# Kernel tuning notes

Measured on AMD Instinct MI355X. Metric: run time of the kernel, lower is better.

Reference implementation:

```python
import jax, jax.numpy as jnp
import numpy as np

EPS = 1e-6

def _rmsnorm(x, w):
    var = jnp.mean(x * x, axis=-1, keepdims=True)
    return w * (x * jax.lax.rsqrt(var + EPS))

def _rope(t, cos, sin):
    # t: [B,S,H,d_k]; cos/sin: [S,d_k/2] -> complex multiply on (even,odd) pairs
    B, S, H, D = t.shape
    tr = t.reshape(B, S, H, D // 2, 2)
    t0, t1 = tr[..., 0], tr[..., 1]
    c = cos[None, :, None, :]
    s = sin[None, :, None, :]
    o0 = t0 * c - t1 * s
    o1 = t0 * s + t1 * c
    return jnp.stack([o0, o1], axis=-1).reshape(B, S, H, D)

def setup_inputs() -> dict:
    key = jax.random.key(0)
    ks = jax.random.split(key, 9)
    B, S, D, H, DFF = 1, 4096, 1024, 16, 4096
    dk = D // H
    hidden = int(2 * DFF / 3)  # 2730, SwiGLU hidden dim
    sc = 0.02
    x = jax.random.normal(ks[0], (B, S, D), jnp.float32)
    # RoPE tables (theta=10000)
    inv_freq = 1.0 / (10000.0 ** (np.arange(0, dk, 2, dtype=np.float32) / dk))
    ang = np.outer(np.arange(S, dtype=np.float32), inv_freq)
    freqs_cos = jnp.asarray(np.cos(ang))
    freqs_sin = jnp.asarray(np.sin(ang))
    # causal additive mask [1,1,S,S]
    mask = jnp.where(np.tril(np.ones((S, S), bool)), 0.0, -1e9).astype(jnp.float32)[None, None]
    Wq = jax.random.normal(ks[1], (D, D), jnp.float32) * sc
    Wk = jax.random.normal(ks[2], (D, D), jnp.float32) * sc
    Wv = jax.random.normal(ks[3], (D, D), jnp.float32) * sc
    Wo = jax.random.normal(ks[4], (D, D), jnp.float32) * sc
    ln1_w = jnp.ones((D,), jnp.float32)
    ln2_w = jnp.ones((D,), jnp.float32)
    w1 = jax.random.normal(ks[5], (D, hidden), jnp.float32) * sc
    w2 = jax.random.normal(ks[6], (hidden, D), jnp.float32) * sc
    w3 = jax.random.normal(ks[7], (D, hidden), jnp.float32) * sc
    return dict(x=x, freqs_cos=freqs_cos, freqs_sin=freqs_sin, mask=mask,
                Wq=Wq, Wk=Wk, Wv=Wv, Wo=Wo, ln1_w=ln1_w, ln2_w=ln2_w,
                w1=w1, w2=w2, w3=w3)

def reference(x, freqs_cos, freqs_sin, mask, Wq, Wk, Wv, Wo, ln1_w, ln2_w, w1, w2, w3):
    B, S, D = x.shape
    H = 16
    dk = D // H
    scale = jnp.sqrt(jnp.float32(dk))
    # attention sublayer (pre-RMSNorm)
    h = _rmsnorm(x, ln1_w)
    Q = (h @ Wq).reshape(B, S, H, dk)
    K = (h @ Wk).reshape(B, S, H, dk)
    V = (h @ Wv).reshape(B, S, H, dk)
    Q = _rope(Q, freqs_cos, freqs_sin)
    K = _rope(K, freqs_cos, freqs_sin)
    scores = jnp.einsum('bshd,bthd->bhst', Q, K) / scale + mask  # [B,H,S,S]
    attn = jax.nn.softmax(scores, axis=-1)
    ctx = jnp.einsum('bhst,bthd->bshd', attn, V).reshape(B, S, D)
    x = x + ctx @ Wo
    # SwiGLU FFN sublayer
    h2 = _rmsnorm(x, ln2_w)
    ff = (jax.nn.silu(h2 @ w1) * (h2 @ w3)) @ w2
    x = x + ff
    return x
```

## Files before the change

### kernel.cpp

```cpp
#include <hip/hip_runtime.h>

#define S_LEN 4096
#define D_MODEL 1024
#define NHEAD 16
#define DK 64
#define HID 2730
#define HIDP 2816
#define QKV_LD 3072

typedef unsigned short u16;
typedef unsigned int u32;
typedef __bf16 bf16x8 __attribute__((ext_vector_type(8)));
typedef float f32x4 __attribute__((ext_vector_type(4)));

#define MFMA16 __builtin_amdgcn_mfma_f32_16x16x32_bf16

__device__ __forceinline__ float b2f(u16 u) {
    return __builtin_bit_cast(float, (u32)u << 16);
}
__device__ __forceinline__ u16 f2b(float f) {
    u32 u = __builtin_bit_cast(u32, f);
    u += 0x7FFF + ((u >> 16) & 1);
    return (u16)(u >> 16);
}
__device__ __forceinline__ u32 pk_trunc(float lo, float hi) {
    return __builtin_amdgcn_perm(__builtin_bit_cast(u32, hi),
                                 __builtin_bit_cast(u32, lo), 0x07060302u);
}
__device__ __forceinline__ void gll16(const u16* g, u16* l) {
    __builtin_amdgcn_global_load_lds(
        (__attribute__((address_space(1))) void*)(g),
        (__attribute__((address_space(3))) void*)(l),
        16, 0, 0);
}

__global__ __launch_bounds__(256)
void rmsnorm_k(const float* __restrict__ x, const float* __restrict__ w,
               u16* __restrict__ out) {
    const int row = blockIdx.x;
    const int tid = threadIdx.x;
    const float4 v = ((const float4*)(x + (size_t)row * D_MODEL))[tid];
    float ss = v.x * v.x + v.y * v.y + v.z * v.z + v.w * v.w;
    for (int o = 32; o; o >>= 1) ss += __shfl_down(ss, o);
    __shared__ float red[4];
    if ((tid & 63) == 0) red[tid >> 6] = ss;
    __syncthreads();
    const float tot = red[0] + red[1] + red[2] + red[3];
    const float rs = rsqrtf(tot * (1.0f / D_MODEL) + 1e-6f);
    const float4 wv = ((const float4*)w)[tid];
    u16* op = out + (size_t)row * D_MODEL + tid * 4;
    u32 p0 = (u32)f2b(v.x * rs * wv.x) | ((u32)f2b(v.y * rs * wv.y) << 16);
    u32 p1 = (u32)f2b(v.z * rs * wv.z) | ((u32)f2b(v.w * rs * wv.w) << 16);
    uint2 pk; pk.x = p0; pk.y = p1;
    *(uint2*)op = pk;
}

__global__ __launch_bounds__(256)
void tcast_k(const float* __restrict__ in, int R, int C,
             u16* __restrict__ out, int outC) {
    __shared__ float t[32][33];
    const int r0 = blockIdx.y * 32;
    const int c0 = blockIdx.x * 32;
    const int tx = threadIdx.x, ty = threadIdx.y;
#pragma unroll
    for (int j = 0; j < 4; ++j) {
        int ir = c0 + ty + j * 8;
        int ic = r0 + tx;
        t[ty + j * 8][tx] = (ir < R && ic < C) ? in[(size_t)ir * C + ic] : 0.0f;
    }
    __syncthreads();
#pragma unroll
    for (int j = 0; j < 4; ++j)
        out[(size_t)(r0 + ty + j * 8) * outC + c0 + tx] = f2b(t[tx][ty + j * 8]);
}

__global__ __launch_bounds__(256)
void packkv_k(const u16* __restrict__ qkv, u16* __restrict__ vt,
              u16* __restrict__ kp) {
    __shared__ u16 t[32][33];
    const int h = blockIdx.z;
    const int t0 = blockIdx.x * 32;
    const int d0 = blockIdx.y * 32;
    const int tx = threadIdx.x, ty = threadIdx.y;
#pragma unroll
    for (int j = 0; j < 4; ++j) {
        const int s = t0 + ty + j * 8;
        t[ty + j * 8][tx] = qkv[(size_t)s * QKV_LD + 2 * D_MODEL + h * DK + d0 + tx];
        kp[((size_t)h * S_LEN + s) * DK + d0 + tx] =
            qkv[(size_t)s * QKV_LD + D_MODEL + h * DK + d0 + tx];
    }
    __syncthreads();
#pragma unroll
    for (int j = 0; j < 4; ++j)
        vt[(size_t)h * DK * S_LEN + (size_t)(d0 + ty + j * 8) * S_LEN + t0 + tx] =
            t[tx][ty + j * 8];
}

__global__ __launch_bounds__(256)
void rope_k(u16* __restrict__ qkv, const float* __restrict__ fc,
            const float* __restrict__ fs) {
    const int idx = blockIdx.x * 256 + threadIdx.x;
    const int s = idx >> 9;
    const int rem = idx & 511;
    const int h = rem >> 5;
    const int i = rem & 31;
    const size_t base = (size_t)s * QKV_LD + h * DK + 2 * i;
    const float c = fc[s * 32 + i], sn = fs[s * 32 + i];
    const float SC = 0.125f * 1.44269504f;
    u16* q = qkv + base;
    u16* k = qkv + base + D_MODEL;
    float t0 = b2f(q[0]), t1 = b2f(q[1]);
    q[0] = f2b((t0 * c - t1 * sn) * SC);
    q[1] = f2b((t0 * sn + t1 * c) * SC);
    t0 = b2f(k[0]); t1 = b2f(k[1]);
    k[0] = f2b(t0 * c - t1 * sn);
    k[1] = f2b(t0 * sn + t1 * c);
}

template <int EPI>
__global__ __launch_bounds__(256)
void gemm128(const u16* __restrict__ A, int lda, const u16* __restrict__ Bt, int ldb,
             void* __restrict__ C, int ldc, int K, const float* __restrict__ resid) {
    const int m0 = blockIdx.y * 128, n0 = blockIdx.x * 128;
    const int tid = threadIdx.x;
    const int wave = tid >> 6, lane = tid & 63;
    const int wr = wave >> 1, wc = wave & 1;
    const int r16 = lane & 15, kq = lane >> 4;

    __shared__ __align__(16) u16 As[128 * 32];
    __shared__ __align__(16) u16 Bs[128 * 32];

    const int srow = tid >> 2, sk = (tid & 3) * 8;
    const u16* ag0 = A + (size_t)(m0 + srow) * lda + sk;
    const u16* ag1 = A + (size_t)(m0 + 64 + srow) * lda + sk;
    const u16* bg0 = Bt + (size_t)(n0 + srow) * ldb + sk;
    const u16* bg1 = Bt + (size_t)(n0 + 64 + srow) * ldb + sk;
    u16* asw = As + wave * 512;
    u16* bsw = Bs + wave * 512;

    f32x4 acc[16];
#pragma unroll
    for (int i = 0; i < 16; ++i) acc[i] = f32x4{0.f, 0.f, 0.f, 0.f};

    for (int k0 = 0; k0 < K; k0 += 32) {
        __syncthreads();
        gll16(ag0 + k0, asw);
        gll16(ag1 + k0, asw + 2048);
        gll16(bg0 + k0, bsw);
        gll16(bg1 + k0, bsw + 2048);
        __syncthreads();
        bf16x8 af[4], bf[4];
#pragma unroll
        for (int mt = 0; mt < 4; ++mt)
            af[mt] = *(const bf16x8*)&As[(wr * 64 + mt * 16 + r16) * 32 + kq * 8];
#pragma unroll
        for (int nt = 0; nt < 4; ++nt)
            bf[nt] = *(const bf16x8*)&Bs[(wc * 64 + nt * 16 + r16) * 32 + kq * 8];
#pragma unroll
        for (int mt = 0; mt < 4; ++mt)
#pragma unroll
            for (int nt = 0; nt < 4; ++nt)
                acc[mt * 4 + nt] = MFMA16(af[mt], bf[nt], acc[mt * 4 + nt], 0, 0, 0);
    }

#pragma unroll
    for (int mt = 0; mt < 4; ++mt) {
#pragma unroll
        for (int nt = 0; nt < 4; ++nt) {
            const int col = n0 + wc * 64 + nt * 16 + r16;
#pragma unroll
            for (int j = 0; j < 4; ++j) {
                const int row = m0 + wr * 64 + mt * 16 + kq * 4 + j;
                if (EPI == 0) {
                    ((u16*)C)[(size_t)row * ldc + col] = f2b(acc[mt * 4 + nt][j]);
                } else {
                    ((float*)C)[(size_t)row * ldc + col] =
                        resid[(size_t)row * ldc + col] + acc[mt * 4 + nt][j];
                }
            }
        }
    }
}

__global__ __launch_bounds__(256)
void gemm64r(const u16* __restrict__ A, int lda, const u16* __restrict__ Bt, int ldb,
             float* __restrict__ C, int ldc, int K, const float* __restrict__ resid) {
    const int m0 = blockIdx.y * 128, n0 = blockIdx.x * 64;
    const int tid = threadIdx.x;
    const int wave = tid >> 6, lane = tid & 63;
    const int r16 = lane & 15, kq = lane >> 4;

    __shared__ __align__(16) u16 As[128 * 32];
    __shared__ __align__(16) u16 Bs[64 * 32];

    const int srow = tid >> 2, sk = (tid & 3) * 8;
    const u16* ag0 = A + (size_t)(m0 + srow) * lda + sk;
    const u16* ag1 = A + (size_t)(m0 + 64 + srow) * lda + sk;
    const u16* bg = Bt + (size_t)(n0 + srow) * ldb + sk;
    u16* asw = As + wave * 512;
    u16* bsw = Bs + wave * 512;

    f32x4 acc[8];
#pragma unroll
    for (int i = 0; i < 8; ++i) acc[i] = f32x4{0.f, 0.f, 0.f, 0.f};

    for (int k0 = 0; k0 < K; k0 += 32) {
        __syncthreads();
        gll16(ag0 + k0, asw);
        gll16(ag1 + k0, asw + 2048);
        gll16(bg + k0, bsw);
        __syncthreads();
        bf16x8 af[2], bf[4];
#pragma unroll
        for (int mt = 0; mt < 2; ++mt)
            af[mt] = *(const bf16x8*)&As[(wave * 32 + mt * 16 + r16) * 32 + kq * 8];
#pragma unroll
        for (int nt = 0; nt < 4; ++nt)
            bf[nt] = *(const bf16x8*)&Bs[(nt * 16 + r16) * 32 + kq * 8];
#pragma unroll
        for (int mt = 0; mt < 2; ++mt)
#pragma unroll
            for (int nt = 0; nt < 4; ++nt)
                acc[mt * 4 + nt] = MFMA16(af[mt], bf[nt], acc[mt * 4 + nt], 0, 0, 0);
    }

#pragma unroll
    for (int mt = 0; mt < 2; ++mt)
#pragma unroll
        for (int nt = 0; nt < 4; ++nt) {
            const int col = n0 + nt * 16 + r16;
#pragma unroll
            for (int j = 0; j < 4; ++j) {
                const int row = m0 + wave * 32 + mt * 16 + kq * 4 + j;
                C[(size_t)row * ldc + col] =
                    resid[(size_t)row * ldc + col] + acc[mt * 4 + nt][j];
            }
        }
}

__global__ __launch_bounds__(256)
void gemm_dual64(const u16* __restrict__ A, int lda,
                 const u16* __restrict__ B1, const u16* __restrict__ B3, int ldb,
                 u16* __restrict__ C, int ldc, int K) {
    const int m0 = blockIdx.y * 128, n0 = blockIdx.x * 64;
    const int tid = threadIdx.x;
    const int wave = tid >> 6, lane = tid & 63;
    const int r16 = lane & 15, kq = lane >> 4;

    __shared__ __align__(16) u16 As[128 * 32];
    __shared__ __align__(16) u16 B1s[64 * 32];
    __shared__ __align__(16) u16 B3s[64 * 32];

    const int srow = tid >> 2, sk = (tid & 3) * 8;
    const u16* ag0 = A + (size_t)(m0 + srow) * lda + sk;
    const u16* ag1 = A + (size_t)(m0 + 64 + srow) * lda + sk;
    const u16* b1g = B1 + (size_t)(n0 + srow) * ldb + sk;
    const u16* b3g = B3 + (size_t)(n0 + srow) * ldb + sk;
    u16* asw = As + wave * 512;
    u16* b1w = B1s + wave * 512;
    u16* b3w = B3s + wave * 512;

    f32x4 acc1[8], acc3[8];
#pragma unroll
    for (int i = 0; i < 8; ++i) {
        acc1[i] = f32x4{0.f, 0.f, 0.f, 0.f};
        acc3[i] = f32x4{0.f, 0.f, 0.f, 0.f};
    }

    for (int k0 = 0; k0 < K; k0 += 32) {
        __syncthreads();
        gll16(ag0 + k0, asw);
        gll16(ag1 + k0, asw + 2048);
        gll16(b1g + k0, b1w);
        gll16(b3g + k0, b3w);
        __syncthreads();
        bf16x8 af[2], b1f[4], b3f[4];
#pragma unroll
        for (int mt = 0; mt < 2; ++mt)
            af[mt] = *(const bf16x8*)&As[(wave * 32 + mt * 16 + r16) * 32 + kq * 8];
#pragma unroll
        for (int nt = 0; nt < 4; ++nt) {
            b1f[nt] = *(const bf16x8*)&B1s[(nt * 16 + r16) * 32 + kq * 8];
            b3f[nt] = *(const bf16x8*)&B3s[(nt * 16 + r16) * 32 + kq * 8];
        }
#pragma unroll
        for (int mt = 0; mt < 2; ++mt)
#pragma unroll
            for (int nt = 0; nt < 4; ++nt) {
                acc1[mt * 4 + nt] = MFMA16(af[mt], b1f[nt], acc1[mt * 4 + nt], 0, 0, 0);
                acc3[mt * 4 + nt] = MFMA16(af[mt], b3f[nt], acc3[mt * 4 + nt], 0, 0, 0);
            }
    }

#pragma unroll
    for (int mt = 0; mt < 2; ++mt)
#pragma unroll
        for (int nt = 0; nt < 4; ++nt) {
            const int col = n0 + nt * 16 + r16;
#pragma unroll
            for (int j = 0; j < 4; ++j) {
                const int row = m0 + wave * 32 + mt * 16 + kq * 4 + j;
                const float v1 = acc1[mt * 4 + nt][j];
                const float v3 = acc3[mt * 4 + nt][j];
                const float sig = 1.0f / (1.0f + __expf(-v1));
                C[(size_t)row * ldc + col] = f2b(v1 * sig * v3);
            }
        }
}

__global__ __launch_bounds__(256)
void flash_k(const u16* __restrict__ qkv, const u16* __restrict__ vt,
             const u16* __restrict__ kp, u16* __restrict__ ctx) {
    const int h = blockIdx.x;
    const int by = blockIdx.y;
    const int hi = by >> 4, lo = by & 15;
    const int base = lo + ((hi >> 1) << 4);
    const int qi = (hi & 1) ? (63 - base) : base;
    const int q0 = qi * 64;
    const int tid = threadIdx.x;
    const int wave = tid >> 6, lane = tid & 63;
    const int r16 = lane & 15, kq = lane >> 4;

    __shared__ __align__(16) u16 Ks[64 * 64];
    __shared__ __align__(16) u16 Vs[64 * 64];
    __shared__ __align__(16) u16 Ps[4][16][72];

    const u16* kb = kp + (size_t)h * S_LEN * DK;
    const u16* vbase = vt + (size_t)h * DK * S_LEN;
    const int srow = tid >> 3;
    const int lcol = ((tid & 7) ^ (srow & 7)) * 8;
    const int qloc = wave * 16 + r16;
    const int sw = r16 & 7;

    const u16* qrow = qkv + (size_t)(q0 + qloc) * QKV_LD + h * DK;
    const bf16x8 qf0 = *(const bf16x8*)(qrow + kq * 8);
    const bf16x8 qf1 = *(const bf16x8*)(qrow + 32 + kq * 8);

    f32x4 o[4];
#pragma unroll
    for (int i = 0; i < 4; ++i) o[i] = f32x4{0.f, 0.f, 0.f, 0.f};
    float lpart = 0.f;

    const int c0 = (kq ^ sw) * 8;
    const int c1 = ((4 ^ kq) ^ sw) * 8;

    for (int t = 0; t <= qi; ++t) {
        const int t0 = t * 64;
        __syncthreads();
#pragma unroll
        for (int i = 0; i < 2; ++i) {
            const int r = srow + i * 32;
            gll16(kb + (size_t)(t0 + r) * DK + lcol, Ks + tid * 8 + i * 2048);
            gll16(vbase + (size_t)r * S_LEN + t0 + lcol, Vs + tid * 8 + i * 2048);
        }
        __syncthreads();

        f32x4 s[4];
#pragma unroll
        for (int nt = 0; nt < 4; ++nt) {
            s[nt] = f32x4{0.f, 0.f, 0.f, 0.f};
            const bf16x8 k0 = *(const bf16x8*)&Ks[(nt * 16 + r16) * 64 + c0];
            s[nt] = MFMA16(k0, qf0, s[nt], 0, 0, 0);
            const bf16x8 k1 = *(const bf16x8*)&Ks[(nt * 16 + r16) * 64 + c1];
            s[nt] = MFMA16(k1, qf1, s[nt], 0, 0, 0);
        }

        float p[16];
#pragma unroll
        for (int nt = 0; nt < 4; ++nt)
#pragma unroll
            for (int j = 0; j < 4; ++j) p[nt * 4 + j] = exp2f(s[nt][j]);
        if (t == qi) {
#pragma unroll
            for (int nt = 0; nt < 4; ++nt)
#pragma unroll
                for (int j = 0; j < 4; ++j)
                    if ((nt * 16 + kq * 4 + j) > qloc) p[nt * 4 + j] = 0.f;
        }
#pragma unroll
        for (int i = 0; i < 16; ++i) lpart += p[i];

#pragma unroll
        for (int nt = 0; nt < 4; ++nt) {
            uint2 pk;
            pk.x = pk_trunc(p[nt * 4 + 0], p[nt * 4 + 1]);
            pk.y = pk_trunc(p[nt * 4 + 2], p[nt * 4 + 3]);
            *(uint2*)&Ps[wave][r16][nt * 16 + kq * 4] = pk;
        }

#pragma unroll
        for (int ks = 0; ks < 2; ++ks) {
            const bf16x8 pf = *(const bf16x8*)&Ps[wave][r16][ks * 32 + kq * 8];
            const int cv = (((ks << 2) ^ kq) ^ sw) * 8;
#pragma unroll
            for (int nt = 0; nt < 4; ++nt) {
                const bf16x8 vf = *(const bf16x8*)&Vs[(nt * 16 + r16) * 64 + cv];
                o[nt] = MFMA16(vf, pf, o[nt], 0, 0, 0);
            }
        }
    }

    lpart += __shfl_xor(lpart, 16);
    lpart += __shfl_xor(lpart, 32);
    const float inv = 1.0f / lpart;
    const size_t row = q0 + qloc;
#pragma unroll
    for (int nt = 0; nt < 4; ++nt) {
        uint2 pk;
        pk.x = (u32)f2b(o[nt][0] * inv) | ((u32)f2b(o[nt][1] * inv) << 16);
        pk.y = (u32)f2b(o[nt][2] * inv) | ((u32)f2b(o[nt][3] * inv) << 16);
        *(uint2*)&ctx[row * D_MODEL + h * DK + nt * 16 + kq * 4] = pk;
    }
}

extern "C" void kernel_launch(void* const* d_in, const int* in_sizes, int n_in,
                              void* d_out, int out_size, void* d_ws, size_t ws_size,
                              hipStream_t stream) {
    const float* x    = (const float*)d_in[0];
    const float* fcos = (const float*)d_in[1];
    const float* fsin = (const float*)d_in[2];
    const float* Wq = (const float*)d_in[4];
    const float* Wk = (const float*)d_in[5];
    const float* Wv = (const float*)d_in[6];
    const float* Wo = (const float*)d_in[7];
    const float* ln1 = (const float*)d_in[8];
    const float* ln2 = (const float*)d_in[9];
    const float* w1 = (const float*)d_in[10];
    const float* w2 = (const float*)d_in[11];
    const float* w3 = (const float*)d_in[12];
    float* out = (float*)d_out;

    char* ws = (char*)d_ws;
    size_t off = 0;
    auto alloc = [&](size_t bytes) -> char* {
        char* p = ws + off;
        off += (bytes + 255) & ~(size_t)255;
        return p;
    };
    u16* hb    = (u16*)alloc((size_t)S_LEN * D_MODEL * 2);
    u16* wqkvt = (u16*)alloc((size_t)QKV_LD * D_MODEL * 2);
    u16* wot   = (u16*)alloc((size_t)D_MODEL * D_MODEL * 2);
    u16* qkvb  = (u16*)alloc((size_t)S_LEN * QKV_LD * 2);
    u16* vt    = (u16*)alloc((size_t)S_LEN * D_MODEL * 2);
    u16* kpack = (u16*)alloc((size_t)S_LEN * D_MODEL * 2);
    u16* ctxb  = (u16*)alloc((size_t)S_LEN * D_MODEL * 2);
    float* x2  = (float*)alloc((size_t)S_LEN * D_MODEL * 4);
    u16* h2b   = (u16*)alloc((size_t)S_LEN * D_MODEL * 2);
    u16* w1t   = (u16*)alloc((size_t)HIDP * D_MODEL * 2);
    u16* w3t   = (u16*)alloc((size_t)HIDP * D_MODEL * 2);
    u16* w2t   = (u16*)alloc((size_t)D_MODEL * HIDP * 2);
    u16* ffb   = (u16*)alloc((size_t)S_LEN * HIDP * 2);

    const dim3 tb32(32, 8);

    tcast_k<<<dim3(32, 32), tb32, 0, stream>>>(Wq, D_MODEL, D_MODEL, wqkvt, D_MODEL);
    tcast_k<<<dim3(32, 32), tb32, 0, stream>>>(Wk, D_MODEL, D_MODEL,
                                               wqkvt + (size_t)D_MODEL * D_MODEL, D_MODEL);
    tcast_k<<<dim3(32, 32), tb32, 0, stream>>>(Wv, D_MODEL, D_MODEL,
                                               wqkvt + (size_t)2 * D_MODEL * D_MODEL, D_MODEL);
    tcast_k<<<dim3(32, 32), tb32, 0, stream>>>(Wo, D_MODEL, D_MODEL, wot, D_MODEL);
    tcast_k<<<dim3(32, HIDP / 32), tb32, 0, stream>>>(w1, D_MODEL, HID, w1t, D_MODEL);
    tcast_k<<<dim3(32, HIDP / 32), tb32, 0, stream>>>(w3, D_MODEL, HID, w3t, D_MODEL);
    tcast_k<<<dim3(HIDP / 32, 32), tb32, 0, stream>>>(w2, HID, D_MODEL, w2t, HIDP);

    rmsnorm_k<<<S_LEN, 256, 0, stream>>>(x, ln1, hb);

    gemm128<0><<<dim3(QKV_LD / 128, S_LEN / 128), 256, 0, stream>>>(
        hb, D_MODEL, wqkvt, D_MODEL, qkvb, QKV_LD, D_MODEL, nullptr);

    rope_k<<<(S_LEN * NHEAD * 32) / 256, 256, 0, stream>>>(qkvb, fcos, fsin);

    packkv_k<<<dim3(S_LEN / 32, DK / 32, NHEAD), tb32, 0, stream>>>(qkvb, vt, kpack);

    flash_k<<<dim3(NHEAD, 64), 256, 0, stream>>>(qkvb, vt, kpack, ctxb);

    gemm64r<<<dim3(D_MODEL / 64, S_LEN / 128), 256, 0, stream>>>(
        ctxb, D_MODEL, wot, D_MODEL, x2, D_MODEL, D_MODEL, x);

    rmsnorm_k<<<S_LEN, 256, 0, stream>>>(x2, ln2, h2b);

    gemm_dual64<<<dim3(HIDP / 64, S_LEN / 128), 256, 0, stream>>>(
        h2b, D_MODEL, w1t, w3t, D_MODEL, ffb, HIDP, D_MODEL);

    gemm64r<<<dim3(D_MODEL / 64, S_LEN / 128), 256, 0, stream>>>(
        ffb, HIDP, w2t, HIDP, out, D_MODEL, HIDP, x2);
}
```

Baseline: 452.0 us.

## Fuse RoPE into K packing and flash Q load, merge weight casts, widen KV tile

The standalone RoPE kernel is removed. K is rotated inside the K/V packing kernel, and Q is rotated and pre-scaled when each flash block loads its Q fragment, which drops one full read-modify-write pass over the QKV buffer. The seven weight transpose-cast launches become a single launch that finds its matrix from the block index. Each flash-attention iteration now stages two 64-wide K/V tiles (128 keys) to halve the barrier count, with a swizzled P scratch layout. In exchange it uses more LDS per block, which can lower occupancy, and on even query tiles it computes a fully masked extra half tile.

Result: faster. 424.2 us (-6.2%).

```diff
diff --git a/kernel.cpp b/kernel.cpp
--- a/kernel.cpp
+++ b/kernel.cpp
@@ -56,11 +56,32 @@
 }
 
 __global__ __launch_bounds__(256)
-void tcast_k(const float* __restrict__ in, int R, int C,
-             u16* __restrict__ out, int outC) {
+void tcast_all(const float* s0, const float* s1, const float* s2,
+               const float* s3, const float* s4, const float* s5,
+               const float* s6, u16* d0, u16* d1, u16* d2, u16* d3,
+               u16* d4, u16* d5, u16* d6) {
+    const float* srcs[7] = {s0, s1, s2, s3, s4, s5, s6};
+    u16* dsts[7] = {d0, d1, d2, d3, d4, d5, d6};
+    const int RR[7] = {1024, 1024, 1024, 1024, 1024, 1024, 2730};
+    const int CC[7] = {1024, 1024, 1024, 1024, 2730, 2730, 1024};
+    const int OC[7] = {1024, 1024, 1024, 1024, 1024, 1024, 2816};
+    const int XD[7] = {32, 32, 32, 32, 32, 32, 88};
+
+    const int bid = blockIdx.x;
+    int seg, start;
+    if (bid < 4096)      { seg = bid >> 10; start = seg << 10; }
+    else if (bid < 6912) { seg = 4; start = 4096; }
+    else if (bid < 9728) { seg = 5; start = 6912; }
+    else                 { seg = 6; start = 9728; }
+    const int local = bid - start;
+    const int bx = local % XD[seg], byy = local / XD[seg];
+    const float* in = srcs[seg];
+    u16* out = dsts[seg];
+    const int R = RR[seg], C = CC[seg], outC = OC[seg];
+
     __shared__ float t[32][33];
-    const int r0 = blockIdx.y * 32;
-    const int c0 = blockIdx.x * 32;
+    const int r0 = byy * 32;
+    const int c0 = bx * 32;
     const int tx = threadIdx.x, ty = threadIdx.y;
 #pragma unroll
     for (int j = 0; j < 4; ++j) {
@@ -75,7 +96,8 @@
 }
 
 __global__ __launch_bounds__(256)
-void packkv_k(const u16* __restrict__ qkv, u16* __restrict__ vt,
+void packkv_k(const u16* __restrict__ qkv, const float* __restrict__ fc,
+              const float* __restrict__ fs, u16* __restrict__ vt,
               u16* __restrict__ kp) {
     __shared__ u16 t[32][33];
     const int h = blockIdx.z;
@@ -83,38 +105,30 @@
     const int d0 = blockIdx.y * 32;
     const int tx = threadIdx.x, ty = threadIdx.y;
 #pragma unroll
-    for (int j = 0; j < 4; ++j) {
-        const int s = t0 + ty + j * 8;
-        t[ty + j * 8][tx] = qkv[(size_t)s * QKV_LD + 2 * D_MODEL + h * DK + d0 + tx];
-        kp[((size_t)h * S_LEN + s) * DK + d0 + tx] =
-            qkv[(size_t)s * QKV_LD + D_MODEL + h * DK + d0 + tx];
-    }
+    for (int j = 0; j < 4; ++j)
+        t[ty + j * 8][tx] =
+            qkv[(size_t)(t0 + ty + j * 8) * QKV_LD + 2 * D_MODEL + h * DK + d0 + tx];
+
+    const int id = ty * 32 + tx;
+    const int sA = t0 + (id >> 3);
+    const int dA = d0 + (id & 7) * 4;
+    uint2 kvp = *(const uint2*)(qkv + (size_t)sA * QKV_LD + D_MODEL + h * DK + dA);
+    const int fi = sA * 32 + (dA >> 1);
+    const float cc0 = fc[fi], ss0 = fs[fi];
+    const float cc1 = fc[fi + 1], ss1 = fs[fi + 1];
+    auto rpk = [](u32 w, float c, float s) -> u32 {
+        const float a = b2f((u16)w), b = b2f((u16)(w >> 16));
+        return (u32)f2b(a * c - b * s) | ((u32)f2b(a * s + b * c) << 16);
+    };
+    kvp.x = rpk(kvp.x, cc0, ss0);
+    kvp.y = rpk(kvp.y, cc1, ss1);
+    *(uint2*)(kp + ((size_t)h * S_LEN + sA) * DK + dA) = kvp;
+
     __syncthreads();
 #pragma unroll
     for (int j = 0; j < 4; ++j)
         vt[(size_t)h * DK * S_LEN + (size_t)(d0 + ty + j * 8) * S_LEN + t0 + tx] =
             t[tx][ty + j * 8];
-}
-
-__global__ __launch_bounds__(256)
-void rope_k(u16* __restrict__ qkv, const float* __restrict__ fc,
-            const float* __restrict__ fs) {
-    const int idx = blockIdx.x * 256 + threadIdx.x;
-    const int s = idx >> 9;
-    const int rem = idx & 511;
-    const int h = rem >> 5;
-    const int i = rem & 31;
-    const size_t base = (size_t)s * QKV_LD + h * DK + 2 * i;
-    const float c = fc[s * 32 + i], sn = fs[s * 32 + i];
-    const float SC = 0.125f * 1.44269504f;
-    u16* q = qkv + base;
-    u16* k = qkv + base + D_MODEL;
-    float t0 = b2f(q[0]), t1 = b2f(q[1]);
-    q[0] = f2b((t0 * c - t1 * sn) * SC);
-    q[1] = f2b((t0 * sn + t1 * c) * SC);
-    t0 = b2f(k[0]); t1 = b2f(k[1]);
-    k[0] = f2b(t0 * c - t1 * sn);
-    k[1] = f2b(t0 * sn + t1 * c);
 }
 
 template <int EPI>
@@ -310,7 +324,8 @@
 
 __global__ __launch_bounds__(256)
 void flash_k(const u16* __restrict__ qkv, const u16* __restrict__ vt,
-             const u16* __restrict__ kp, u16* __restrict__ ctx) {
+             const u16* __restrict__ kp, const float* __restrict__ fc,
+             const float* __restrict__ fs, u16* __restrict__ ctx) {
     const int h = blockIdx.x;
     const int by = blockIdx.y;
     const int hi = by >> 4, lo = by & 15;
@@ -321,81 +336,122 @@
     const int wave = tid >> 6, lane = tid & 63;
     const int r16 = lane & 15, kq = lane >> 4;
 
-    __shared__ __align__(16) u16 Ks[64 * 64];
-    __shared__ __align__(16) u16 Vs[64 * 64];
-    __shared__ __align__(16) u16 Ps[4][16][72];
+    __shared__ __align__(16) u16 KsA[64 * 64];
+    __shared__ __align__(16) u16 KsB[64 * 64];
+    __shared__ __align__(16) u16 VsA[64 * 64];
+    __shared__ __align__(16) u16 VsB[64 * 64];
+    __shared__ __align__(16) u16 Ps[4 * 16 * 64];
 
     const u16* kb = kp + (size_t)h * S_LEN * DK;
-    const u16* vbase = vt + (size_t)h * DK * S_LEN;
+    const u16* vb = vt + (size_t)h * DK * S_LEN;
     const int srow = tid >> 3;
     const int lcol = ((tid & 7) ^ (srow & 7)) * 8;
     const int qloc = wave * 16 + r16;
+    const int qglob = q0 + qloc;
     const int sw = r16 & 7;
-
-    const u16* qrow = qkv + (size_t)(q0 + qloc) * QKV_LD + h * DK;
-    const bf16x8 qf0 = *(const bf16x8*)(qrow + kq * 8);
-    const bf16x8 qf1 = *(const bf16x8*)(qrow + 32 + kq * 8);
+    const int c0 = (kq ^ sw) * 8;
+    const int c1 = ((4 ^ kq) ^ sw) * 8;
+    const int psw = r16 & 14;
+    u16* psrow = Ps + wave * 1024 + r16 * 64;
+
+    const float SC = 0.125f * 1.44269504f;
+    const u16* qrow = qkv + (size_t)qglob * QKV_LD + h * DK;
+    uint4 uq0 = *(const uint4*)(qrow + kq * 8);
+    uint4 uq1 = *(const uint4*)(qrow + 32 + kq * 8);
+    const float4 c0v = *(const float4*)(fc + qglob * 32 + kq * 4);
+    const float4 s0v = *(const float4*)(fs + qglob * 32 + kq * 4);
+    const float4 c1v = *(const float4*)(fc + qglob * 32 + 16 + kq * 4);
+    const float4 s1v = *(const float4*)(fs + qglob * 32 + 16 + kq * 4);
+    auto rp = [SC](u32 w, float c, float s) -> u32 {
+        const float a = b2f((u16)w), b = b2f((u16)(w >> 16));
+        return (u32)f2b((a * c - b * s) * SC) |
+               ((u32)f2b((a * s + b * c) * SC) << 16);
+    };
+    uq0.x = rp(uq0.x, c0v.x, s0v.x); uq0.y = rp(uq0.y, c0v.y, s0v.y);
+    uq0.z = rp(uq0.z, c0v.z, s0v.z); uq0.w = rp(uq0.w, c0v.w, s0v.w);
+    uq1.x = rp(uq1.x, c1v.x, s1v.x); uq1.y = rp(uq1.y, c1v.y, s1v.y);
+    uq1.z = rp(uq1.z, c1v.z, s1v.z); uq1.w = rp(uq1.w, c1v.w, s1v.w);
+    const bf16x8 qf0 = __builtin_bit_cast(bf16x8, uq0);
+    const bf16x8 qf1 = __builtin_bit_cast(bf16x8, uq1);
 
     f32x4 o[4];
 #pragma unroll
     for (int i = 0; i < 4; ++i) o[i] = f32x4{0.f, 0.f, 0.f, 0.f};
     float lpart = 0.f;
-
-    const int c0 = (kq ^ sw) * 8;
-    const int c1 = ((4 ^ kq) ^ sw) * 8;
-
-    for (int t = 0; t <= qi; ++t) {
-        const int t0 = t * 64;
+    const int T = (qi + 2) >> 1;
+
+    for (int t = 0; t < T; ++t) {
+        const int t0 = t * 128;
         __syncthreads();
 #pragma unroll
         for (int i = 0; i < 2; ++i) {
             const int r = srow + i * 32;
-            gll16(kb + (size_t)(t0 + r) * DK + lcol, Ks + tid * 8 + i * 2048);
-            gll16(vbase + (size_t)r * S_LEN + t0 + lcol, Vs + tid * 8 + i * 2048);
-        }
-        __syncthreads();
-
-        f32x4 s[4];
+            gll16(kb + (size_t)(t0 + r) * DK + lcol, KsA + tid * 8 + i * 2048);
+            gll16(kb + (size_t)(t0 + 64 + r) * DK + lcol, KsB + tid * 8 + i * 2048);
+            gll16(vb + (size_t)r * S_LEN + t0 + lcol, VsA + tid * 8 + i * 2048);
+            gll16(vb + (size_t)r * S_LEN + t0 + 64 + lcol, VsB + tid * 8 + i * 2048);
+        }
+        __syncthreads();
+
+        f32x4 s[8];
 #pragma unroll
         for (int nt = 0; nt < 4; ++nt) {
             s[nt] = f32x4{0.f, 0.f, 0.f, 0.f};
-            const bf16x8 k0 = *(const bf16x8*)&Ks[(nt * 16 + r16) * 64 + c0];
+            const bf16x8 k0 = *(const bf16x8*)&KsA[(nt * 16 + r16) * 64 + c0];
             s[nt] = MFMA16(k0, qf0, s[nt], 0, 0, 0);
-            const bf16x8 k1 = *(const bf16x8*)&Ks[(nt * 16 + r16) * 64 + c1];
+            const bf16x8 k1 = *(const bf16x8*)&KsA[(nt * 16 + r16) * 64 + c1];
             s[nt] = MFMA16(k1, qf1, s[nt], 0, 0, 0);
         }
-
-        float p[16];
-#pragma unroll
-        for (int nt = 0; nt < 4; ++nt)
-#pragma unroll
-            for (int j = 0; j < 4; ++j) p[nt * 4 + j] = exp2f(s[nt][j]);
-        if (t == qi) {
+#pragma unroll
+        for (int nt = 0; nt < 4; ++nt) {
+            s[4 + nt] = f32x4{0.f, 0.f, 0.f, 0.f};
+            const bf16x8 k0 = *(const bf16x8*)&KsB[(nt * 16 + r16) * 64 + c0];
+            s[4 + nt] = MFMA16(k0, qf0, s[4 + nt], 0, 0, 0);
+            const bf16x8 k1 = *(const bf16x8*)&KsB[(nt * 16 + r16) * 64 + c1];
+            s[4 + nt] = MFMA16(k1, qf1, s[4 + nt], 0, 0, 0);
+        }
+
+        const bool lastT = (t == T - 1);
+#pragma unroll
+        for (int p = 0; p < 2; ++p) {
+            float pr[16];
 #pragma unroll
             for (int nt = 0; nt < 4; ++nt)
 #pragma unroll
                 for (int j = 0; j < 4; ++j)
-                    if ((nt * 16 + kq * 4 + j) > qloc) p[nt * 4 + j] = 0.f;
-        }
-#pragma unroll
-        for (int i = 0; i < 16; ++i) lpart += p[i];
-
-#pragma unroll
-        for (int nt = 0; nt < 4; ++nt) {
-            uint2 pk;
-            pk.x = pk_trunc(p[nt * 4 + 0], p[nt * 4 + 1]);
-            pk.y = pk_trunc(p[nt * 4 + 2], p[nt * 4 + 3]);
-            *(uint2*)&Ps[wave][r16][nt * 16 + kq * 4] = pk;
-        }
-
-#pragma unroll
-        for (int ks = 0; ks < 2; ++ks) {
-            const bf16x8 pf = *(const bf16x8*)&Ps[wave][r16][ks * 32 + kq * 8];
-            const int cv = (((ks << 2) ^ kq) ^ sw) * 8;
+                    pr[nt * 4 + j] = exp2f(s[p * 4 + nt][j]);
+            if (lastT) {
+                const int kvb = t0 + p * 64;
+#pragma unroll
+                for (int nt = 0; nt < 4; ++nt)
+#pragma unroll
+                    for (int j = 0; j < 4; ++j)
+                        if ((kvb + nt * 16 + kq * 4 + j) > qglob)
+                            pr[nt * 4 + j] = 0.f;
+            }
+#pragma unroll
+            for (int i = 0; i < 16; ++i) lpart += pr[i];
+
 #pragma unroll
             for (int nt = 0; nt < 4; ++nt) {
-                const bf16x8 vf = *(const bf16x8*)&Vs[(nt * 16 + r16) * 64 + cv];
-                o[nt] = MFMA16(vf, pf, o[nt], 0, 0, 0);
+                uint2 pk;
+                pk.x = pk_trunc(pr[nt * 4 + 0], pr[nt * 4 + 1]);
+                pk.y = pk_trunc(pr[nt * 4 + 2], pr[nt * 4 + 3]);
+                *(uint2*)&psrow[((nt * 4 + kq) ^ psw) * 4] = pk;
+            }
+
+#pragma unroll
+            for (int ks = 0; ks < 2; ++ks) {
+                const bf16x8 pf =
+                    *(const bf16x8*)&psrow[((8 * ks + 2 * kq) ^ psw) * 4];
+                const int cv = (((ks << 2) ^ kq) ^ sw) * 8;
+#pragma unroll
+                for (int nt = 0; nt < 4; ++nt) {
+                    const bf16x8 vf = p
+                        ? *(const bf16x8*)&VsB[(nt * 16 + r16) * 64 + cv]
+                        : *(const bf16x8*)&VsA[(nt * 16 + r16) * 64 + cv];
+                    o[nt] = MFMA16(vf, pf, o[nt], 0, 0, 0);
+                }
             }
         }
     }
@@ -403,7 +459,7 @@
     lpart += __shfl_xor(lpart, 16);
     lpart += __shfl_xor(lpart, 32);
     const float inv = 1.0f / lpart;
-    const size_t row = q0 + qloc;
+    const size_t row = qglob;
 #pragma unroll
     for (int nt = 0; nt < 4; ++nt) {
         uint2 pk;
@@ -453,26 +509,20 @@
 
     const dim3 tb32(32, 8);
 
-    tcast_k<<<dim3(32, 32), tb32, 0, stream>>>(Wq, D_MODEL, D_MODEL, wqkvt, D_MODEL);
-    tcast_k<<<dim3(32, 32), tb32, 0, stream>>>(Wk, D_MODEL, D_MODEL,
-                                               wqkvt + (size_t)D_MODEL * D_MODEL, D_MODEL);
-    tcast_k<<<dim3(32, 32), tb32, 0, stream>>>(Wv, D_MODEL, D_MODEL,
-                                               wqkvt + (size_t)2 * D_MODEL * D_MODEL, D_MODEL);
-    tcast_k<<<dim3(32, 32), tb32, 0, stream>>>(Wo, D_MODEL, D_MODEL, wot, D_MODEL);
-    tcast_k<<<dim3(32, HIDP / 32), tb32, 0, stream>>>(w1, D_MODEL, HID, w1t, D_MODEL);
-    tcast_k<<<dim3(32, HIDP / 32), tb32, 0, stream>>>(w3, D_MODEL, HID, w3t, D_MODEL);
-    tcast_k<<<dim3(HIDP / 32, 32), tb32, 0, stream>>>(w2, HID, D_MODEL, w2t, HIDP);
+    tcast_all<<<12544, tb32, 0, stream>>>(
+        Wq, Wk, Wv, Wo, w1, w3, w2,
+        wqkvt, wqkvt + (size_t)D_MODEL * D_MODEL,
+        wqkvt + (size_t)2 * D_MODEL * D_MODEL, wot, w1t, w3t, w2t);
 
     rmsnorm_k<<<S_LEN, 256, 0, stream>>>(x, ln1, hb);
 
     gemm128<0><<<dim3(QKV_LD / 128, S_LEN / 128), 256, 0, stream>>>(
         hb, D_MODEL, wqkvt, D_MODEL, qkvb, QKV_LD, D_MODEL, nullptr);
 
-    rope_k<<<(S_LEN * NHEAD * 32) / 256, 256, 0, stream>>>(qkvb, fcos, fsin);
-
-    packkv_k<<<dim3(S_LEN / 32, DK / 32, NHEAD), tb32, 0, stream>>>(qkvb, vt, kpack);
-
-    flash_k<<<dim3(NHEAD, 64), 256, 0, stream>>>(qkvb, vt, kpack, ctxb);
+    packkv_k<<<dim3(S_LEN / 32, DK / 32, NHEAD), tb32, 0, stream>>>(
+        qkvb, fcos, fsin, vt, kpack);
+
+    flash_k<<<dim3(NHEAD, 64), 256, 0, stream>>>(qkvb, vt, kpack, fcos, fsin, ctxb);
 
     gemm64r<<<dim3(D_MODEL / 64, S_LEN / 128), 256, 0, stream>>>(
         ctxb, D_MODEL, wot, D_MODEL, x2, D_MODEL, D_MODEL, x);
```
